# Kernel tuning notes

Hardware: AMD Instinct MI355X
Metric: run time of the kernel (lower is better)

Reference implementation:

```python
import jax, jax.numpy as jnp
import numpy as np
import math

B, T, C, H, DFF = 4, 2048, 1024, 16, 4096
HD = C // H
EPS = 1e-5


def _layernorm(x, g, b):
    mu = jnp.mean(x, axis=-1, keepdims=True)
    var = jnp.var(x, axis=-1, keepdims=True)
    return (x - mu) * jax.lax.rsqrt(var + EPS) * g + b


def _new_gelu(x):
    # 0.5*x*(1+tanh(sqrt(2/pi)*(x+0.044715*x^3)))
    c = math.sqrt(2.0 / math.pi)
    return 0.5 * x * (1.0 + jnp.tanh(c * (x + 0.044715 * x ** 3)))


def setup_inputs() -> dict:
    key = jax.random.key(0)
    ks = jax.random.split(key, 12)
    s = lambda fan_in: 1.0 / math.sqrt(fan_in)
    return {
        "x": jax.random.normal(ks[0], (B, T, C), jnp.float32),
        "ln1_g": jnp.ones((C,), jnp.float32),
        "ln1_b": jnp.zeros((C,), jnp.float32),
        "w_qkv": jax.random.normal(ks[1], (C, 3 * C), jnp.float32) * s(C),
        "b_qkv": jnp.zeros((3 * C,), jnp.float32),
        "w_o": jax.random.normal(ks[2], (C, C), jnp.float32) * s(C),
        "b_o": jnp.zeros((C,), jnp.float32),
        "ln2_g": jnp.ones((C,), jnp.float32),
        "ln2_b": jnp.zeros((C,), jnp.float32),
        "w_fc": jax.random.normal(ks[3], (C, DFF), jnp.float32) * s(C),
        "b_fc": jnp.zeros((DFF,), jnp.float32),
        "w_proj": jax.random.normal(ks[4], (DFF, C), jnp.float32) * s(DFF),
        "b_proj": jnp.zeros((C,), jnp.float32),
    }


def reference(x, ln1_g, ln1_b, w_qkv, b_qkv, w_o, b_o, ln2_g, ln2_b, w_fc, b_fc, w_proj, b_proj):
    # --- attention sub-block ---
    h = _layernorm(x, ln1_g, ln1_b)
    qkv = h @ w_qkv + b_qkv                                  # (B,T,3C)
    q, k, v = jnp.split(qkv, 3, axis=-1)
    q = q.reshape(B, T, H, HD).transpose(0, 2, 1, 3)          # (B,H,T,hd)
    k = k.reshape(B, T, H, HD).transpose(0, 2, 1, 3)
    v = v.reshape(B, T, H, HD).transpose(0, 2, 1, 3)
    scores = jnp.einsum("bhqd,bhkd->bhqk", q, k) / math.sqrt(HD)
    causal = jnp.tril(jnp.ones((T, T), jnp.bool_))            # (T,T)
    scores = jnp.where(causal[None, None], scores, -jnp.inf)
    probs = jax.nn.softmax(scores, axis=-1)
    attn = jnp.einsum("bhqk,bhkd->bhqd", probs, v)
    attn = attn.transpose(0, 2, 1, 3).reshape(B, T, C)
    x = x + attn @ w_o + b_o
    # --- MLP sub-block ---
    h2 = _layernorm(x, ln2_g, ln2_b)
    x = x + _new_gelu(h2 @ w_fc + b_fc) @ w_proj + b_proj
    return x
```

## Files before the change

kernel.cpp:

```cpp
#include <hip/hip_runtime.h>
#include <hip/hip_bf16.h>

using bf16 = __hip_bfloat16;
typedef __attribute__((ext_vector_type(8))) short bf16x8;
typedef __attribute__((ext_vector_type(4))) float f32x4;
typedef __attribute__((ext_vector_type(16))) float f32x16;

#define LOG2E 1.4426950408889634f

__device__ inline short f2b(float f) {
  __hip_bfloat16 h = __float2bfloat16(f);
  return *reinterpret_cast<short*>(&h);
}
__device__ inline float b2f(short s) {
  unsigned int u = ((unsigned int)(unsigned short)s) << 16;
  float f;
  __builtin_memcpy(&f, &u, 4);
  return f;
}
__device__ inline unsigned pk2(float a, float b) {
  return (unsigned)(unsigned short)f2b(a) |
         ((unsigned)(unsigned short)f2b(b) << 16);
}

__global__ __launch_bounds__(256) void transpose_cast_kernel(
    const float* __restrict__ in, bf16* __restrict__ out, int K, int N) {
  __shared__ float tile[32][33];
  int tx = threadIdx.x & 31;
  int ty = threadIdx.x >> 5;
  int n0 = blockIdx.x * 32, k0 = blockIdx.y * 32;
#pragma unroll
  for (int i = 0; i < 4; i++)
    tile[ty + i * 8][tx] = in[(size_t)(k0 + ty + i * 8) * N + n0 + tx];
  __syncthreads();
#pragma unroll
  for (int i = 0; i < 4; i++)
    out[(size_t)(n0 + ty + i * 8) * K + k0 + tx] =
        __float2bfloat16(tile[tx][ty + i * 8]);
}

__global__ __launch_bounds__(256) void transpose_v_kernel(
    const bf16* __restrict__ qkv, bf16* __restrict__ vt) {
  __shared__ short tile[64][66];
  const int bh = blockIdx.y;
  const int b = bh >> 4, h = bh & 15;
  const int t0 = blockIdx.x * 64;
  const int tid = threadIdx.x;
  const int r = tid >> 3, c8 = (tid & 7) * 8;
#pragma unroll
  for (int p = 0; p < 2; p++) {
    int t = r + p * 32;
    bf16x8 v = *(const bf16x8*)&qkv[(size_t)(b * 2048 + t0 + t) * 3072 + 2048 +
                                    h * 64 + c8];
#pragma unroll
    for (int i = 0; i < 8; i++) tile[t][c8 + i] = v[i];
  }
  __syncthreads();
#pragma unroll
  for (int p = 0; p < 2; p++) {
    int d = r + p * 32;
    int tt = c8;
    bf16x8 o;
#pragma unroll
    for (int i = 0; i < 8; i++) o[i] = tile[tt + i][d];
    *(bf16x8*)&vt[(size_t)(bh * 64 + d) * 2048 + t0 + tt] = o;
  }
}

__global__ __launch_bounds__(256) void ln_kernel(
    const float* __restrict__ x, const float* __restrict__ g,
    const float* __restrict__ b, bf16* __restrict__ out) {
  int row = blockIdx.x;
  const float4 v = ((const float4*)(x + (size_t)row * 1024))[threadIdx.x];
  float s = v.x + v.y + v.z + v.w;
  float ss = v.x * v.x + v.y * v.y + v.z * v.z + v.w * v.w;
#pragma unroll
  for (int off = 1; off < 64; off <<= 1) {
    s += __shfl_xor(s, off);
    ss += __shfl_xor(ss, off);
  }
  __shared__ float red[2][4];
  int w = threadIdx.x >> 6, lane = threadIdx.x & 63;
  if (lane == 0) { red[0][w] = s; red[1][w] = ss; }
  __syncthreads();
  s = red[0][0] + red[0][1] + red[0][2] + red[0][3];
  ss = red[1][0] + red[1][1] + red[1][2] + red[1][3];
  float mu = s * (1.0f / 1024.0f);
  float var = ss * (1.0f / 1024.0f) - mu * mu;
  float rstd = rsqrtf(var + 1e-5f);
  const float4 gv = ((const float4*)g)[threadIdx.x];
  const float4 bv = ((const float4*)b)[threadIdx.x];
  short4 o4;
  o4.x = f2b((v.x - mu) * rstd * gv.x + bv.x);
  o4.y = f2b((v.y - mu) * rstd * gv.y + bv.y);
  o4.z = f2b((v.z - mu) * rstd * gv.z + bv.z);
  o4.w = f2b((v.w - mu) * rstd * gv.w + bv.w);
  ((short4*)out)[(size_t)row * 256 + threadIdx.x] = o4;
}

template <int MLO, int NLO>
__device__ inline void quad_mfma(f32x4 (&acc)[4][4], bf16x8 (&af)[2][2],
                                 bf16x8 (&bf)[2][2]) {
  __builtin_amdgcn_s_barrier();
  asm volatile("s_waitcnt lgkmcnt(0)" ::: "memory");
  __builtin_amdgcn_sched_barrier(0);
  __builtin_amdgcn_s_setprio(1);
#pragma unroll
  for (int mm = 0; mm < 2; mm++)
#pragma unroll
    for (int nn = 0; nn < 2; nn++)
#pragma unroll
      for (int ks = 0; ks < 2; ks++)
        acc[MLO + mm][NLO + nn] = __builtin_amdgcn_mfma_f32_16x16x32_bf16(
            af[mm][ks], bf[nn][ks], acc[MLO + mm][NLO + nn], 0, 0, 0);
  __builtin_amdgcn_s_setprio(0);
  __builtin_amdgcn_s_barrier();
}

template <int EPI>
__global__ __launch_bounds__(512, 1) void gemm_bt8_kernel(
    const bf16* __restrict__ A, const bf16* __restrict__ Bt,
    const float* __restrict__ bias, const float* __restrict__ res,
    void* __restrict__ out, int M, int N, int K) {
  __shared__ short As[2][128 * 64];
  __shared__ short Bs[2][256 * 64];
  const int tid = threadIdx.x;
  const int lane = tid & 63, wid = tid >> 6;
  const int wr = wid >> 2, wc = wid & 3;

  const int nwg = gridDim.x;
  const int gy = M >> 7;
  const int flat = blockIdx.x;
  const int sw = (flat & 7) * (nwg >> 3) + (flat >> 3);
  const int bcol = sw / gy, brow = sw % gy;

  const int nk = K >> 6;

  auto stA = [&](int kt, int buf) {
#pragma unroll
    for (int r = 0; r < 2; r++) {
      const int row = tid >> 3;
      const int chs = (tid & 7) ^ (row & 7);
      const bf16* src =
          A + (size_t)(brow * 128 + r * 64 + row) * K + kt * 64 + chs * 8;
      __builtin_amdgcn_global_load_lds(
          (const __attribute__((address_space(1))) unsigned int*)src,
          (__attribute__((address_space(3))) unsigned int*)
              &As[buf][(r * 64 + wid * 8) * 64],
          16, 0, 0);
    }
  };
  auto stB = [&](int kt, int buf, int r0) {
#pragma unroll
    for (int rr = 0; rr < 2; rr++) {
      const int r = r0 + rr;
      const int row = tid >> 3;
      const int chs = (tid & 7) ^ (row & 7);
      const bf16* src =
          Bt + (size_t)(bcol * 256 + r * 64 + row) * K + kt * 64 + chs * 8;
      __builtin_amdgcn_global_load_lds(
          (const __attribute__((address_space(1))) unsigned int*)src,
          (__attribute__((address_space(3))) unsigned int*)
              &Bs[buf][(r * 64 + wid * 8) * 64],
          16, 0, 0);
    }
  };

  f32x4 acc[4][4] = {};
  bf16x8 af[2][2], bf0[2][2], bf1[2][2];
  int cur = 0;

  auto rdA = [&](int mh) {
#pragma unroll
    for (int mm = 0; mm < 2; mm++)
#pragma unroll
      for (int ks = 0; ks < 2; ks++) {
        const int row = wr * 64 + (mh * 2 + mm) * 16 + (lane & 15);
        const int ch = (ks * 4 + (lane >> 4)) ^ (row & 7);
        af[mm][ks] = *(const bf16x8*)&As[cur][row * 64 + ch * 8];
      }
  };
  auto rdB = [&](bf16x8(&bf)[2][2], int nh) {
#pragma unroll
    for (int nn = 0; nn < 2; nn++)
#pragma unroll
      for (int ks = 0; ks < 2; ks++) {
        const int row = wc * 64 + (nh * 2 + nn) * 16 + (lane & 15);
        const int ch = (ks * 4 + (lane >> 4)) ^ (row & 7);
        bf[nn][ks] = *(const bf16x8*)&Bs[cur][row * 64 + ch * 8];
      }
  };

  stA(0, 0);
  stB(0, 0, 0);
  stB(0, 0, 2);
  stA(1, 1);
  asm volatile("s_waitcnt vmcnt(2)" ::: "memory");
  __builtin_amdgcn_s_barrier();

  for (int t = 0; t < nk; t++) {
    cur = t & 1;
    const int nxt = cur ^ 1;
    rdA(0);
    rdB(bf0, 0);
    if (t + 1 < nk) stB(t + 1, nxt, 0);
    quad_mfma<0, 0>(acc, af, bf0);
    rdB(bf1, 1);
    if (t + 1 < nk) stB(t + 1, nxt, 2);
    quad_mfma<0, 2>(acc, af, bf1);
    rdA(1);
    quad_mfma<2, 2>(acc, af, bf1);
    if (t + 2 < nk) {
      stA(t + 2, cur);
      asm volatile("s_waitcnt vmcnt(2)" ::: "memory");
    } else if (t + 1 < nk) {
      asm volatile("s_waitcnt vmcnt(0)" ::: "memory");
    }
    quad_mfma<2, 0>(acc, af, bf0);
  }

#pragma unroll
  for (int m = 0; m < 4; m++)
#pragma unroll
    for (int n = 0; n < 4; n++) {
      int gr0 = brow * 128 + wr * 64 + m * 16 + (lane >> 4) * 4;
      int gc = bcol * 256 + wc * 64 + n * 16 + (lane & 15);
      float bia = bias[gc];
#pragma unroll
      for (int j = 0; j < 4; j++) {
        float v = acc[m][n][j] + bia;
        size_t idx = (size_t)(gr0 + j) * N + gc;
        if constexpr (EPI == 0) {
          ((bf16*)out)[idx] = __float2bfloat16(v);
        } else if constexpr (EPI == 1) {
          ((float*)out)[idx] = v + res[idx];
        } else {
          float u = 0.7978845608028654f * (v + 0.044715f * v * v * v);
          float t2 = exp2f(u * (2.0f * LOG2E));
          float th = 1.0f - 2.0f / (t2 + 1.0f);
          ((bf16*)out)[idx] = __float2bfloat16(0.5f * v * (1.0f + th));
        }
      }
    }
}

__global__ __launch_bounds__(256) void attn_kernel(
    const bf16* __restrict__ qkv, const bf16* __restrict__ vt,
    bf16* __restrict__ attn) {
  const int bh = blockIdx.x;
  const int qt = blockIdx.y;
  const int b = bh >> 4, h = bh & 15;
  const int tid = threadIdx.x, w = tid >> 6, lane = tid & 63;
  const int col = lane & 31;
  const int hi = lane >> 5;

  __shared__ short Kl[64 * 64];
  __shared__ short Vl[64 * 64];

  const int qbase = qt * 128 + w * 32;
  const int qglob = qbase + col;
  const size_t qrow = (size_t)(b * 2048 + qglob);

  bf16x8 qf[4];
#pragma unroll
  for (int dks = 0; dks < 4; dks++) {
    bf16x8 raw =
        *(const bf16x8*)&qkv[qrow * 3072 + h * 64 + dks * 16 + hi * 8];
#pragma unroll
    for (int i = 0; i < 8; i++) qf[dks][i] = f2b(b2f(raw[i]) * 0.125f);
  }

  f32x16 ot[2] = {};
  float m = -1e30f, l = 0.0f;

  const int ktend = qt * 2 + 1;
  for (int kt = 0; kt <= ktend; kt++) {
    const int kv0 = kt * 64;
    __syncthreads();
#pragma unroll
    for (int j = 0; j < 2; j++) {
      int c = (j * 4 + w) * 64 + lane;
      int row = c >> 3;
      int sw8 = ((c & 7) ^ (row & 7)) * 8;
      const bf16* gk =
          qkv + (size_t)(b * 2048 + kv0 + row) * 3072 + 1024 + h * 64 + sw8;
      __builtin_amdgcn_global_load_lds(
          (const __attribute__((address_space(1))) unsigned int*)gk,
          (__attribute__((address_space(3))) unsigned int*)(Kl + (j * 4 + w) * 512),
          16, 0, 0);
      const bf16* gv = vt + (size_t)(bh * 64 + row) * 2048 + kv0 + sw8;
      __builtin_amdgcn_global_load_lds(
          (const __attribute__((address_space(1))) unsigned int*)gv,
          (__attribute__((address_space(3))) unsigned int*)(Vl + (j * 4 + w) * 512),
          16, 0, 0);
    }
    __syncthreads();

    if (kv0 <= qbase + 31) {
      f32x16 st[2] = {};
#pragma unroll
      for (int s = 0; s < 2; s++) {
        int kvrow = s * 32 + col;
        int swz = kvrow & 7;
#pragma unroll
        for (int dks = 0; dks < 4; dks++) {
          int ch = (dks * 2 + hi) ^ swz;
          bf16x8 kf = *(const bf16x8*)&Kl[kvrow * 64 + ch * 8];
          st[s] = __builtin_amdgcn_mfma_f32_32x32x16_bf16(kf, qf[dks], st[s],
                                                          0, 0, 0);
        }
      }
      if (kv0 + 63 > qbase) {
#pragma unroll
        for (int s = 0; s < 2; s++)
#pragma unroll
          for (int r = 0; r < 16; r++) {
            int kv = kv0 + s * 32 + (r & 3) + 8 * (r >> 2) + 4 * hi;
            if (kv > qglob) st[s][r] = -1e30f;
          }
      }
      float pmax = -1e30f;
#pragma unroll
      for (int s = 0; s < 2; s++)
#pragma unroll
        for (int r = 0; r < 16; r++) pmax = fmaxf(pmax, st[s][r]);
      pmax = fmaxf(pmax, __shfl_xor(pmax, 32));
      float mnew = fmaxf(m, pmax);
      float corr = exp2f((m - mnew) * LOG2E);
      m = mnew;
      float rs = 0.0f;
#pragma unroll
      for (int s = 0; s < 2; s++)
#pragma unroll
        for (int r = 0; r < 16; r++) {
          float pv = exp2f((st[s][r] - mnew) * LOG2E);
          st[s][r] = pv;
          rs += pv;
        }
      rs += __shfl_xor(rs, 32);
      l = l * corr + rs;
#pragma unroll
      for (int s = 0; s < 2; s++)
#pragma unroll
        for (int r = 0; r < 16; r++) ot[s][r] *= corr;

#pragma unroll
      for (int sub = 0; sub < 2; sub++) {
#pragma unroll
        for (int kl = 0; kl < 2; kl++) {
          unsigned A0 = pk2(st[sub][kl * 8 + 0], st[sub][kl * 8 + 1]);
          unsigned A1 = pk2(st[sub][kl * 8 + 2], st[sub][kl * 8 + 3]);
          unsigned B0 = pk2(st[sub][kl * 8 + 4], st[sub][kl * 8 + 5]);
          unsigned B1 = pk2(st[sub][kl * 8 + 6], st[sub][kl * 8 + 7]);
          unsigned sA0 = (unsigned)__shfl_xor((int)A0, 32);
          unsigned sA1 = (unsigned)__shfl_xor((int)A1, 32);
          unsigned sB0 = (unsigned)__shfl_xor((int)B0, 32);
          unsigned sB1 = (unsigned)__shfl_xor((int)B1, 32);
          union { unsigned u[4]; bf16x8 v; } pf;
          pf.u[0] = hi ? sB0 : A0;
          pf.u[1] = hi ? sB1 : A1;
          pf.u[2] = hi ? B0 : sA0;
          pf.u[3] = hi ? B1 : sA1;
          int ks = sub * 2 + kl;
#pragma unroll
          for (int ds = 0; ds < 2; ds++) {
            int drow = ds * 32 + col;
            int ch = (ks * 2 + hi) ^ (drow & 7);
            bf16x8 vf = *(const bf16x8*)&Vl[drow * 64 + ch * 8];
            ot[ds] = __builtin_amdgcn_mfma_f32_32x32x16_bf16(vf, pf.v, ot[ds],
                                                             0, 0, 0);
          }
        }
      }
    }
  }

  float rl = 1.0f / l;
#pragma unroll
  for (int ds = 0; ds < 2; ds++)
#pragma unroll
    for (int j = 0; j < 4; j++) {
      ushort4 o4;
      o4.x = (unsigned short)f2b(ot[ds][4 * j + 0] * rl);
      o4.y = (unsigned short)f2b(ot[ds][4 * j + 1] * rl);
      o4.z = (unsigned short)f2b(ot[ds][4 * j + 2] * rl);
      o4.w = (unsigned short)f2b(ot[ds][4 * j + 3] * rl);
      *(ushort4*)&attn[qrow * 1024 + h * 64 + 32 * ds + 8 * j + 4 * hi] = o4;
    }
}

extern "C" void kernel_launch(void* const* d_in, const int* in_sizes, int n_in,
                              void* d_out, int out_size, void* d_ws,
                              size_t ws_size, hipStream_t stream) {
  (void)in_sizes; (void)n_in; (void)out_size; (void)ws_size;
  const float* x      = (const float*)d_in[0];
  const float* ln1_g  = (const float*)d_in[1];
  const float* ln1_b  = (const float*)d_in[2];
  const float* w_qkv  = (const float*)d_in[3];
  const float* b_qkv  = (const float*)d_in[4];
  const float* w_o    = (const float*)d_in[5];
  const float* b_o    = (const float*)d_in[6];
  const float* ln2_g  = (const float*)d_in[7];
  const float* ln2_b  = (const float*)d_in[8];
  const float* w_fc   = (const float*)d_in[9];
  const float* b_fc   = (const float*)d_in[10];
  const float* w_proj = (const float*)d_in[11];
  const float* b_proj = (const float*)d_in[12];
  float* out = (float*)d_out;

  char* ws = (char*)d_ws;
  bf16* wt_qkv  = (bf16*)(ws + 0);
  bf16* wt_o    = (bf16*)(ws + 6291456);
  bf16* wt_fc   = (bf16*)(ws + 8388608);
  bf16* wt_proj = (bf16*)(ws + 16777216);
  float* x1     = (float*)(ws + 25165824);
  bf16* vtb     = (bf16*)(ws + 25165824);
  bf16* slotA   = (bf16*)(ws + 58720256);
  bf16* qkvb    = (bf16*)(ws + 75497472);
  bf16* gbuf    = (bf16*)(ws + 75497472);

  dim3 blk(256);
  transpose_cast_kernel<<<dim3(3072 / 32, 1024 / 32), blk, 0, stream>>>(
      w_qkv, wt_qkv, 1024, 3072);
  transpose_cast_kernel<<<dim3(1024 / 32, 1024 / 32), blk, 0, stream>>>(
      w_o, wt_o, 1024, 1024);
  transpose_cast_kernel<<<dim3(4096 / 32, 1024 / 32), blk, 0, stream>>>(
      w_fc, wt_fc, 1024, 4096);
  transpose_cast_kernel<<<dim3(1024 / 32, 4096 / 32), blk, 0, stream>>>(
      w_proj, wt_proj, 4096, 1024);

  ln_kernel<<<8192, blk, 0, stream>>>(x, ln1_g, ln1_b, slotA);
  gemm_bt8_kernel<0><<<dim3(768), dim3(512), 0, stream>>>(
      slotA, wt_qkv, b_qkv, nullptr, qkvb, 8192, 3072, 1024);
  transpose_v_kernel<<<dim3(32, 64), blk, 0, stream>>>(qkvb, vtb);
  attn_kernel<<<dim3(64, 16), blk, 0, stream>>>(qkvb, vtb, slotA);
  gemm_bt8_kernel<1><<<dim3(256), dim3(512), 0, stream>>>(
      slotA, wt_o, b_o, x, x1, 8192, 1024, 1024);
  ln_kernel<<<8192, blk, 0, stream>>>(x1, ln2_g, ln2_b, slotA);
  gemm_bt8_kernel<2><<<dim3(1024), dim3(512), 0, stream>>>(
      slotA, wt_fc, b_fc, nullptr, gbuf, 8192, 4096, 1024);
  gemm_bt8_kernel<1><<<dim3(256), dim3(512), 0, stream>>>(
      gbuf, wt_proj, b_proj, x1, out, 8192, 1024, 4096);
}
```

Measured before the change: 480.5 us.

## Use 256x256 GEMM tiles with split-K for N=1024 GEMMs and fused residual-LN

Replaces the 128x256 GEMM with a 256x256 tile kernel, which doubles per-block data reuse and uses a simpler double-buffered loop. The two N=1024 GEMMs (attention output and MLP projection) now split K in two so there are enough blocks to fill the GPU. Their partial sums are combined in a fused kernel that adds bias and residual, and for the first one also applies LayerNorm 2. This costs extra fp32 partial-sum traffic and two added elementwise passes, and the simpler pipeline waits on vmcnt(0) each iteration, which may expose load latency.

```diff
diff --git a/kernel.cpp b/kernel.cpp
--- a/kernel.cpp
+++ b/kernel.cpp
@@ -98,51 +98,96 @@
   ((short4*)out)[(size_t)row * 256 + threadIdx.x] = o4;
 }
 
-template <int MLO, int NLO>
-__device__ inline void quad_mfma(f32x4 (&acc)[4][4], bf16x8 (&af)[2][2],
-                                 bf16x8 (&bf)[2][2]) {
-  __builtin_amdgcn_s_barrier();
-  asm volatile("s_waitcnt lgkmcnt(0)" ::: "memory");
-  __builtin_amdgcn_sched_barrier(0);
-  __builtin_amdgcn_s_setprio(1);
-#pragma unroll
-  for (int mm = 0; mm < 2; mm++)
-#pragma unroll
-    for (int nn = 0; nn < 2; nn++)
-#pragma unroll
-      for (int ks = 0; ks < 2; ks++)
-        acc[MLO + mm][NLO + nn] = __builtin_amdgcn_mfma_f32_16x16x32_bf16(
-            af[mm][ks], bf[nn][ks], acc[MLO + mm][NLO + nn], 0, 0, 0);
-  __builtin_amdgcn_s_setprio(0);
-  __builtin_amdgcn_s_barrier();
+__global__ __launch_bounds__(256) void fused_ln_kernel(
+    const float* __restrict__ p0, const float* __restrict__ p1,
+    const float* __restrict__ bo, const float* __restrict__ x,
+    const float* __restrict__ g, const float* __restrict__ bln,
+    float* __restrict__ x1, bf16* __restrict__ h2) {
+  int row = blockIdx.x;
+  size_t base = (size_t)row * 256 + threadIdx.x;
+  float4 a = ((const float4*)p0)[base];
+  float4 c = ((const float4*)p1)[base];
+  float4 xr = ((const float4*)x)[base];
+  float4 bo4 = ((const float4*)bo)[threadIdx.x];
+  float4 v;
+  v.x = a.x + c.x + xr.x + bo4.x;
+  v.y = a.y + c.y + xr.y + bo4.y;
+  v.z = a.z + c.z + xr.z + bo4.z;
+  v.w = a.w + c.w + xr.w + bo4.w;
+  ((float4*)x1)[base] = v;
+  float s = v.x + v.y + v.z + v.w;
+  float ss = v.x * v.x + v.y * v.y + v.z * v.z + v.w * v.w;
+#pragma unroll
+  for (int off = 1; off < 64; off <<= 1) {
+    s += __shfl_xor(s, off);
+    ss += __shfl_xor(ss, off);
+  }
+  __shared__ float red[2][4];
+  int w = threadIdx.x >> 6, lane = threadIdx.x & 63;
+  if (lane == 0) { red[0][w] = s; red[1][w] = ss; }
+  __syncthreads();
+  s = red[0][0] + red[0][1] + red[0][2] + red[0][3];
+  ss = red[1][0] + red[1][1] + red[1][2] + red[1][3];
+  float mu = s * (1.0f / 1024.0f);
+  float var = ss * (1.0f / 1024.0f) - mu * mu;
+  float rstd = rsqrtf(var + 1e-5f);
+  const float4 gv = ((const float4*)g)[threadIdx.x];
+  const float4 bv = ((const float4*)bln)[threadIdx.x];
+  short4 o4;
+  o4.x = f2b((v.x - mu) * rstd * gv.x + bv.x);
+  o4.y = f2b((v.y - mu) * rstd * gv.y + bv.y);
+  o4.z = f2b((v.z - mu) * rstd * gv.z + bv.z);
+  o4.w = f2b((v.w - mu) * rstd * gv.w + bv.w);
+  ((short4*)h2)[base] = o4;
+}
+
+__global__ __launch_bounds__(256) void fused_add_kernel(
+    float* __restrict__ out, const float* __restrict__ q1,
+    const float* __restrict__ x1, const float* __restrict__ bp, int n4) {
+  for (int i = blockIdx.x * 256 + threadIdx.x; i < n4; i += gridDim.x * 256) {
+    float4 a = ((const float4*)out)[i];
+    float4 c = ((const float4*)q1)[i];
+    float4 xr = ((const float4*)x1)[i];
+    float4 b4 = ((const float4*)bp)[i & 255];
+    float4 v;
+    v.x = a.x + c.x + xr.x + b4.x;
+    v.y = a.y + c.y + xr.y + b4.y;
+    v.z = a.z + c.z + xr.z + b4.z;
+    v.w = a.w + c.w + xr.w + b4.w;
+    ((float4*)out)[i] = v;
+  }
 }
 
 template <int EPI>
-__global__ __launch_bounds__(512, 1) void gemm_bt8_kernel(
+__global__ __launch_bounds__(512, 1) void gemm256_kernel(
     const bf16* __restrict__ A, const bf16* __restrict__ Bt,
-    const float* __restrict__ bias, const float* __restrict__ res,
-    void* __restrict__ out, int M, int N, int K) {
-  __shared__ short As[2][128 * 64];
+    const float* __restrict__ bias, float* __restrict__ out0,
+    float* __restrict__ out1, void* __restrict__ outv, int M, int N, int Kfull,
+    int Ksub, int ntiles) {
+  __shared__ short As[2][256 * 64];
   __shared__ short Bs[2][256 * 64];
   const int tid = threadIdx.x;
   const int lane = tid & 63, wid = tid >> 6;
   const int wr = wid >> 2, wc = wid & 3;
 
   const int nwg = gridDim.x;
-  const int gy = M >> 7;
   const int flat = blockIdx.x;
   const int sw = (flat & 7) * (nwg >> 3) + (flat >> 3);
-  const int bcol = sw / gy, brow = sw % gy;
-
-  const int nk = K >> 6;
+  const int kq = sw / ntiles;
+  const int tile = sw % ntiles;
+  const int gy = M >> 8;
+  const int bcol = tile / gy, brow = tile % gy;
+  const int koff = kq * Ksub;
+  const int nk = Ksub >> 6;
+
+  const int srow = tid >> 3;
+  const int schs = (tid & 7) ^ (srow & 7);
 
   auto stA = [&](int kt, int buf) {
 #pragma unroll
-    for (int r = 0; r < 2; r++) {
-      const int row = tid >> 3;
-      const int chs = (tid & 7) ^ (row & 7);
-      const bf16* src =
-          A + (size_t)(brow * 128 + r * 64 + row) * K + kt * 64 + chs * 8;
+    for (int r = 0; r < 4; r++) {
+      const bf16* src = A + (size_t)(brow * 256 + r * 64 + srow) * Kfull +
+                        koff + kt * 64 + schs * 8;
       __builtin_amdgcn_global_load_lds(
           (const __attribute__((address_space(1))) unsigned int*)src,
           (__attribute__((address_space(3))) unsigned int*)
@@ -150,14 +195,11 @@
           16, 0, 0);
     }
   };
-  auto stB = [&](int kt, int buf, int r0) {
-#pragma unroll
-    for (int rr = 0; rr < 2; rr++) {
-      const int r = r0 + rr;
-      const int row = tid >> 3;
-      const int chs = (tid & 7) ^ (row & 7);
-      const bf16* src =
-          Bt + (size_t)(bcol * 256 + r * 64 + row) * K + kt * 64 + chs * 8;
+  auto stB = [&](int kt, int buf) {
+#pragma unroll
+    for (int r = 0; r < 4; r++) {
+      const bf16* src = Bt + (size_t)(bcol * 256 + r * 64 + srow) * Kfull +
+                        koff + kt * 64 + schs * 8;
       __builtin_amdgcn_global_load_lds(
           (const __attribute__((address_space(1))) unsigned int*)src,
           (__attribute__((address_space(3))) unsigned int*)
@@ -166,79 +208,99 @@
     }
   };
 
-  f32x4 acc[4][4] = {};
-  bf16x8 af[2][2], bf0[2][2], bf1[2][2];
-  int cur = 0;
-
-  auto rdA = [&](int mh) {
-#pragma unroll
-    for (int mm = 0; mm < 2; mm++)
+  f32x4 acc[8][4] = {};
+  bf16x8 af[4][2], bfr[4][2];
+
+  auto rdB = [&](int cur) {
+#pragma unroll
+    for (int nn = 0; nn < 4; nn++)
 #pragma unroll
       for (int ks = 0; ks < 2; ks++) {
-        const int row = wr * 64 + (mh * 2 + mm) * 16 + (lane & 15);
+        const int row = wc * 64 + nn * 16 + (lane & 15);
+        const int ch = (ks * 4 + (lane >> 4)) ^ (row & 7);
+        bfr[nn][ks] = *(const bf16x8*)&Bs[cur][row * 64 + ch * 8];
+      }
+  };
+  auto rdA = [&](int cur, int mh) {
+#pragma unroll
+    for (int mm = 0; mm < 4; mm++)
+#pragma unroll
+      for (int ks = 0; ks < 2; ks++) {
+        const int row = wr * 128 + mh * 64 + mm * 16 + (lane & 15);
         const int ch = (ks * 4 + (lane >> 4)) ^ (row & 7);
         af[mm][ks] = *(const bf16x8*)&As[cur][row * 64 + ch * 8];
       }
   };
-  auto rdB = [&](bf16x8(&bf)[2][2], int nh) {
-#pragma unroll
-    for (int nn = 0; nn < 2; nn++)
-#pragma unroll
-      for (int ks = 0; ks < 2; ks++) {
-        const int row = wc * 64 + (nh * 2 + nn) * 16 + (lane & 15);
-        const int ch = (ks * 4 + (lane >> 4)) ^ (row & 7);
-        bf[nn][ks] = *(const bf16x8*)&Bs[cur][row * 64 + ch * 8];
-      }
-  };
 
   stA(0, 0);
-  stB(0, 0, 0);
-  stB(0, 0, 2);
-  stA(1, 1);
-  asm volatile("s_waitcnt vmcnt(2)" ::: "memory");
+  stB(0, 0);
+  asm volatile("s_waitcnt vmcnt(0)" ::: "memory");
   __builtin_amdgcn_s_barrier();
 
   for (int t = 0; t < nk; t++) {
-    cur = t & 1;
-    const int nxt = cur ^ 1;
-    rdA(0);
-    rdB(bf0, 0);
-    if (t + 1 < nk) stB(t + 1, nxt, 0);
-    quad_mfma<0, 0>(acc, af, bf0);
-    rdB(bf1, 1);
-    if (t + 1 < nk) stB(t + 1, nxt, 2);
-    quad_mfma<0, 2>(acc, af, bf1);
-    rdA(1);
-    quad_mfma<2, 2>(acc, af, bf1);
-    if (t + 2 < nk) {
-      stA(t + 2, cur);
-      asm volatile("s_waitcnt vmcnt(2)" ::: "memory");
-    } else if (t + 1 < nk) {
-      asm volatile("s_waitcnt vmcnt(0)" ::: "memory");
-    }
-    quad_mfma<2, 0>(acc, af, bf0);
-  }
-
-#pragma unroll
-  for (int m = 0; m < 4; m++)
+    const int cur = t & 1, nxt = cur ^ 1;
+    rdB(cur);
+    rdA(cur, 0);
+    if (t + 1 < nk) {
+      stA(t + 1, nxt);
+      stB(t + 1, nxt);
+    }
+    __builtin_amdgcn_s_barrier();
+    asm volatile("s_waitcnt lgkmcnt(0)" ::: "memory");
+    __builtin_amdgcn_sched_barrier(0);
+    __builtin_amdgcn_s_setprio(1);
+#pragma unroll
+    for (int mm = 0; mm < 4; mm++)
+#pragma unroll
+      for (int nn = 0; nn < 4; nn++)
+#pragma unroll
+        for (int ks = 0; ks < 2; ks++)
+          acc[mm][nn] = __builtin_amdgcn_mfma_f32_16x16x32_bf16(
+              af[mm][ks], bfr[nn][ks], acc[mm][nn], 0, 0, 0);
+    __builtin_amdgcn_s_setprio(0);
+    __builtin_amdgcn_s_barrier();
+    rdA(cur, 1);
+    asm volatile("s_waitcnt lgkmcnt(0)" ::: "memory");
+    __builtin_amdgcn_sched_barrier(0);
+    __builtin_amdgcn_s_setprio(1);
+#pragma unroll
+    for (int mm = 0; mm < 4; mm++)
+#pragma unroll
+      for (int nn = 0; nn < 4; nn++)
+#pragma unroll
+        for (int ks = 0; ks < 2; ks++)
+          acc[4 + mm][nn] = __builtin_amdgcn_mfma_f32_16x16x32_bf16(
+              af[mm][ks], bfr[nn][ks], acc[4 + mm][nn], 0, 0, 0);
+    __builtin_amdgcn_s_setprio(0);
+    if (t + 1 < nk) asm volatile("s_waitcnt vmcnt(0)" ::: "memory");
+    __builtin_amdgcn_s_barrier();
+  }
+
+#pragma unroll
+  for (int m = 0; m < 8; m++)
 #pragma unroll
     for (int n = 0; n < 4; n++) {
-      int gr0 = brow * 128 + wr * 64 + m * 16 + (lane >> 4) * 4;
+      int gr0 = brow * 256 + wr * 128 + m * 16 + (lane >> 4) * 4;
       int gc = bcol * 256 + wc * 64 + n * 16 + (lane & 15);
-      float bia = bias[gc];
-#pragma unroll
-      for (int j = 0; j < 4; j++) {
-        float v = acc[m][n][j] + bia;
-        size_t idx = (size_t)(gr0 + j) * N + gc;
-        if constexpr (EPI == 0) {
-          ((bf16*)out)[idx] = __float2bfloat16(v);
-        } else if constexpr (EPI == 1) {
-          ((float*)out)[idx] = v + res[idx];
-        } else {
-          float u = 0.7978845608028654f * (v + 0.044715f * v * v * v);
-          float t2 = exp2f(u * (2.0f * LOG2E));
-          float th = 1.0f - 2.0f / (t2 + 1.0f);
-          ((bf16*)out)[idx] = __float2bfloat16(0.5f * v * (1.0f + th));
+      if constexpr (EPI == 3) {
+        float* po = kq ? out1 : out0;
+#pragma unroll
+        for (int j = 0; j < 4; j++)
+          po[(size_t)(gr0 + j) * N + gc] = acc[m][n][j];
+      } else {
+        float bia = bias[gc];
+#pragma unroll
+        for (int j = 0; j < 4; j++) {
+          float v = acc[m][n][j] + bia;
+          size_t idx = (size_t)(gr0 + j) * N + gc;
+          if constexpr (EPI == 0) {
+            ((bf16*)outv)[idx] = __float2bfloat16(v);
+          } else {
+            float u = 0.7978845608028654f * (v + 0.044715f * v * v * v);
+            float t2 = exp2f(u * (2.0f * LOG2E));
+            float th = 1.0f - 2.0f / (t2 + 1.0f);
+            ((bf16*)outv)[idx] = __float2bfloat16(0.5f * v * (1.0f + th));
+          }
         }
       }
     }
@@ -409,15 +471,19 @@
   float* out = (float*)d_out;
 
   char* ws = (char*)d_ws;
-  bf16* wt_qkv  = (bf16*)(ws + 0);
-  bf16* wt_o    = (bf16*)(ws + 6291456);
-  bf16* wt_fc   = (bf16*)(ws + 8388608);
-  bf16* wt_proj = (bf16*)(ws + 16777216);
-  float* x1     = (float*)(ws + 25165824);
-  bf16* vtb     = (bf16*)(ws + 25165824);
-  bf16* slotA   = (bf16*)(ws + 58720256);
-  bf16* qkvb    = (bf16*)(ws + 75497472);
-  bf16* gbuf    = (bf16*)(ws + 75497472);
+  const size_t MB = 1048576;
+  float* x1     = (float*)(ws + 0);
+  bf16* slotA   = (bf16*)(ws + 32 * MB);
+  bf16* wt_qkv  = (bf16*)(ws + 48 * MB);
+  bf16* wt_o    = (bf16*)(ws + 54 * MB);
+  bf16* wt_fc   = (bf16*)(ws + 56 * MB);
+  bf16* wt_proj = (bf16*)(ws + 64 * MB);
+  bf16* qkvb    = (bf16*)(ws + 72 * MB);
+  bf16* vtb     = (bf16*)(ws + 120 * MB);
+  float* p0     = (float*)(ws + 72 * MB);
+  float* p1     = (float*)(ws + 104 * MB);
+  bf16* gbuf    = (bf16*)(ws + 72 * MB);
+  float* q1     = (float*)(ws + 32 * MB);
 
   dim3 blk(256);
   transpose_cast_kernel<<<dim3(3072 / 32, 1024 / 32), blk, 0, stream>>>(
@@ -430,15 +496,19 @@
       w_proj, wt_proj, 4096, 1024);
 
   ln_kernel<<<8192, blk, 0, stream>>>(x, ln1_g, ln1_b, slotA);
-  gemm_bt8_kernel<0><<<dim3(768), dim3(512), 0, stream>>>(
-      slotA, wt_qkv, b_qkv, nullptr, qkvb, 8192, 3072, 1024);
+  gemm256_kernel<0><<<dim3(384), dim3(512), 0, stream>>>(
+      slotA, wt_qkv, b_qkv, nullptr, nullptr, qkvb, 8192, 3072, 1024, 1024,
+      384);
   transpose_v_kernel<<<dim3(32, 64), blk, 0, stream>>>(qkvb, vtb);
   attn_kernel<<<dim3(64, 16), blk, 0, stream>>>(qkvb, vtb, slotA);
-  gemm_bt8_kernel<1><<<dim3(256), dim3(512), 0, stream>>>(
-      slotA, wt_o, b_o, x, x1, 8192, 1024, 1024);
-  ln_kernel<<<8192, blk, 0, stream>>>(x1, ln2_g, ln2_b, slotA);
-  gemm_bt8_kernel<2><<<dim3(1024), dim3(512), 0, stream>>>(
-      slotA, wt_fc, b_fc, nullptr, gbuf, 8192, 4096, 1024);
-  gemm_bt8_kernel<1><<<dim3(256), dim3(512), 0, stream>>>(
-      gbuf, wt_proj, b_proj, x1, out, 8192, 1024, 4096);
-}
+  gemm256_kernel<3><<<dim3(256), dim3(512), 0, stream>>>(
+      slotA, wt_o, nullptr, p0, p1, nullptr, 8192, 1024, 1024, 512, 128);
+  fused_ln_kernel<<<8192, blk, 0, stream>>>(p0, p1, b_o, x, ln2_g, ln2_b, x1,
+                                            slotA);
+  gemm256_kernel<2><<<dim3(512), dim3(512), 0, stream>>>(
+      slotA, wt_fc, b_fc, nullptr, nullptr, gbuf, 8192, 4096, 1024, 1024, 512);
+  gemm256_kernel<3><<<dim3(256), dim3(512), 0, stream>>>(
+      gbuf, wt_proj, nullptr, out, q1, nullptr, 8192, 1024, 4096, 2048, 128);
+  fused_add_kernel<<<dim3(2048), blk, 0, stream>>>(out, q1, x1, b_proj,
+                                                   2097152);
+}
```

Result: faster. 444.7 us (-7.5%).
